# Optimization experiments

Measured on AMD Instinct MI355X. Metric: run time of the kernel, lower is better.

Reference implementation:

```python
import jax, jax.numpy as jnp
import numpy as np


def setup_inputs() -> dict:
    key = jax.random.key(0)
    bs, n_heads, ch, length = 4, 8, 64, 2048
    width = 3 * n_heads * ch  # 1536
    qkv = jax.random.normal(key, (bs, width, length), dtype=jnp.float32)
    return {"qkv": qkv, "n_heads": n_heads}


def reference(qkv, n_heads):
    bs, width, length = qkv.shape
    ch = width // (3 * n_heads)
    # reshape to (bs*heads, 3*ch, length) then split into q, k, v of (B, ch, L)
    qkv_r = qkv.reshape(bs * n_heads, 3 * ch, length)
    q, k, v = qkv_r[:, :ch], qkv_r[:, ch:2 * ch], qkv_r[:, 2 * ch:]
    scale = ch ** (-0.5)
    # weight = bmm(q^T, k) * scale -> (B, L_q, L_k)
    weight = jnp.einsum('bct,bcs->bts', q, k) * scale
    weight = jax.nn.softmax(weight.astype(jnp.float32), axis=-1).astype(qkv.dtype)
    # a = bmm(v, weight^T) -> (B, ch, L)
    a = jnp.einsum('bcs,bts->bct', v, weight)
    return a.reshape(bs, n_heads * ch, length)
```

## Files before the change

kernel.cpp:

```cpp
#include <hip/hip_runtime.h>

typedef __bf16 bf16;
typedef __attribute__((ext_vector_type(8)))  __bf16 bf16x8;
typedef __attribute__((ext_vector_type(16))) float  f32x16;

#define LEN   2048
#define CH    64
#define HEADS 32

union PackU { unsigned u[4]; bf16x8 v; };

static __device__ inline unsigned pack2(float lo, float hi) {
  union { bf16 h[2]; unsigned u; } p;
  p.h[0] = (bf16)lo; p.h[1] = (bf16)hi;
  return p.u;
}

static __device__ inline void async_cp16(const bf16* g, bf16* l) {
  __builtin_amdgcn_global_load_lds(
      (const __attribute__((address_space(1))) void*)g,
      (__attribute__((address_space(3))) void*)l, 16, 0, 0);
}

__global__ __launch_bounds__(256) void prep_kernel(const float* __restrict__ qkv,
                                                   bf16* __restrict__ ws) {
  __shared__ float tile[64][65];
  const int tIdx = blockIdx.x;
  const int g    = blockIdx.y;
  const int tid  = threadIdx.x;
  const int s0   = tIdx * 64;
  const float* K = qkv + (g * 192 + 64)  * LEN;
  const float* V = qkv + (g * 192 + 128) * LEN;

  {
    const int c0 = tid >> 6, s = tid & 63;
#pragma unroll
    for (int i = 0; i < 16; ++i) {
      const int c = c0 + i * 4;
      tile[c][s] = K[c * LEN + s0 + s];
    }
  }
  __syncthreads();

  bf16* dst = ws + ((size_t)g * 32 + tIdx) * 8192;
#pragma unroll
  for (int it = 0; it < 2; ++it) {
    const int c2  = tid + it * 256;
    const int row = c2 >> 3, cx = c2 & 7;
    const int cb  = (cx ^ (row & 7)) * 8;
    bf16x8 o;
#pragma unroll
    for (int j = 0; j < 8; ++j) o[j] = (bf16)tile[cb + j][row];
    *(bf16x8*)(dst + c2 * 8) = o;
  }
#pragma unroll
  for (int it = 0; it < 2; ++it) {
    const int c2  = tid + it * 256;
    const int row = c2 >> 3, k8 = c2 & 7;
    const int pa  = 32 * (k8 >> 2) + 8 * ((k8 >> 1) & 1) + 4 * (k8 & 1);
    const float* src = V + row * LEN + s0 + pa;
    const float4 a = *(const float4*)src;
    const float4 b = *(const float4*)(src + 16);
    bf16x8 o;
    o[0] = (bf16)a.x; o[1] = (bf16)a.y; o[2] = (bf16)a.z; o[3] = (bf16)a.w;
    o[4] = (bf16)b.x; o[5] = (bf16)b.y; o[6] = (bf16)b.z; o[7] = (bf16)b.w;
    *(bf16x8*)(dst + 4096 + c2 * 8) = o;
  }
}

__global__ __launch_bounds__(256, 2) void attn_kernel(const float* __restrict__ qkv,
                                                      const bf16* __restrict__ ws,
                                                      float* __restrict__ out) {
  __shared__ __align__(16) unsigned char lds_raw[35392];
  bf16* stg = (bf16*)lds_raw;

  const int tid  = threadIdx.x;
  const int lane = tid & 63;
  const int w    = tid >> 6;
  const int wg   = w & 1;
  const int sg   = w >> 1;
  const int n    = lane & 31;
  const int h    = lane >> 5;
  const int g    = blockIdx.x & 31;
  const int jb   = blockIdx.x >> 5;
  const int t0   = jb * 128 + wg * 64;

  const bf16* wsg    = ws + (size_t)g * (32 * 8192);
  const bf16* tiles0 = wsg + (size_t)(sg * 16) * 8192;

  auto stage = [&](int i) {
    const bf16* src = tiles0 + i * 8192;
    bf16* dstp = stg + (sg * 2 + (i & 1)) * 4096;
#pragma unroll
    for (int it = 0; it < 4; ++it) {
      const int chunk = wg * 256 + it * 64 + lane;
      async_cp16(src + chunk * 8, dstp + chunk * 8);
    }
  };
  stage(0);

  const float qs = 0.125f * 1.44269504088896340736f;
  const float* Q = qkv + g * (192 * LEN);
  bf16x8 qf[2][4];
#pragma unroll
  for (int e = 0; e < 2; ++e)
#pragma unroll
    for (int kb = 0; kb < 4; ++kb)
#pragma unroll
      for (int jj = 0; jj < 8; ++jj)
        qf[e][kb][jj] = (bf16)(Q[(kb * 16 + h * 8 + jj) * LEN + t0 + e * 32 + n] * qs);

  f32x16 o_acc[2][2];
#pragma unroll
  for (int e = 0; e < 2; ++e)
#pragma unroll
    for (int mb = 0; mb < 2; ++mb)
#pragma unroll
      for (int r = 0; r < 16; ++r) o_acc[e][mb][r] = 0.f;
  float l_acc[2] = {0.f, 0.f};

  for (int i = 0; i < 16; ++i) {
    __syncthreads();
    if (i < 15) stage(i + 1);

    const bf16* vt = tiles0 + i * 8192 + 4096;
    bf16x8 vf[4][2];
#pragma unroll
    for (int kbs = 0; kbs < 4; ++kbs)
#pragma unroll
      for (int mbo = 0; mbo < 2; ++mbo)
        vf[kbs][mbo] = *(const bf16x8*)(vt + (mbo * 32 + n) * 64 + (kbs * 2 + h) * 8);

    const bf16* ktl = stg + (sg * 2 + (i & 1)) * 4096;

    f32x16 sf[2][2];
#pragma unroll
    for (int e = 0; e < 2; ++e)
#pragma unroll
      for (int mb = 0; mb < 2; ++mb)
#pragma unroll
        for (int r = 0; r < 16; ++r) sf[e][mb][r] = 0.f;
#pragma unroll
    for (int kb = 0; kb < 4; ++kb)
#pragma unroll
      for (int mb = 0; mb < 2; ++mb) {
        const bf16x8 a = *(const bf16x8*)(ktl + (mb * 32 + n) * 64 + (((kb * 2 + h) ^ (n & 7)) * 8));
        sf[0][mb] = __builtin_amdgcn_mfma_f32_32x32x16_bf16(a, qf[0][kb], sf[0][mb], 0, 0, 0);
        sf[1][mb] = __builtin_amdgcn_mfma_f32_32x32x16_bf16(a, qf[1][kb], sf[1][mb], 0, 0, 0);
      }

    PackU frag[2][4];
#pragma unroll
    for (int e = 0; e < 2; ++e) {
      float ls = 0.f;
#pragma unroll
      for (int mb = 0; mb < 2; ++mb)
#pragma unroll
        for (int u = 0; u < 4; ++u) {
          const float p0 = __builtin_amdgcn_exp2f(sf[e][mb][4 * u + 0]);
          const float p1 = __builtin_amdgcn_exp2f(sf[e][mb][4 * u + 1]);
          const float p2 = __builtin_amdgcn_exp2f(sf[e][mb][4 * u + 2]);
          const float p3 = __builtin_amdgcn_exp2f(sf[e][mb][4 * u + 3]);
          ls += (p0 + p1) + (p2 + p3);
          const int kb   = 2 * mb + (u & 1);
          const int base = 2 * (u >> 1);
          frag[e][kb].u[base]     = pack2(p0, p1);
          frag[e][kb].u[base + 1] = pack2(p2, p3);
        }
      l_acc[e] += ls;
    }

#pragma unroll
    for (int kbs = 0; kbs < 4; ++kbs)
#pragma unroll
      for (int mbo = 0; mbo < 2; ++mbo) {
        o_acc[0][mbo] = __builtin_amdgcn_mfma_f32_32x32x16_bf16(vf[kbs][mbo], frag[0][kbs].v, o_acc[0][mbo], 0, 0, 0);
        o_acc[1][mbo] = __builtin_amdgcn_mfma_f32_32x32x16_bf16(vf[kbs][mbo], frag[1][kbs].v, o_acc[1][mbo], 0, 0, 0);
      }
  }

  float lt[2];
#pragma unroll
  for (int e = 0; e < 2; ++e) lt[e] = l_acc[e] + __shfl_xor(l_acc[e], 32);

  float* ebuf = (float*)lds_raw;
  float* lbuf = (float*)(lds_raw + 34816);

  __syncthreads();
  if (sg == 1) {
#pragma unroll
    for (int e = 0; e < 2; ++e)
#pragma unroll
      for (int mbo = 0; mbo < 2; ++mbo)
#pragma unroll
        for (int u = 0; u < 4; ++u) {
          float4 st;
          st.x = o_acc[e][mbo][4 * u + 0];
          st.y = o_acc[e][mbo][4 * u + 1];
          st.z = o_acc[e][mbo][4 * u + 2];
          st.w = o_acc[e][mbo][4 * u + 3];
          *(float4*)&ebuf[wg * 4352 + (e * 32 + n) * 68 + mbo * 32 + 8 * u + 4 * h] = st;
        }
    if (h == 0) {
      lbuf[wg * 64 + n]      = lt[0];
      lbuf[wg * 64 + 32 + n] = lt[1];
    }
  }
  __syncthreads();
  if (sg == 0) {
    float inv[2];
#pragma unroll
    for (int e = 0; e < 2; ++e) inv[e] = 1.0f / (lt[e] + lbuf[wg * 64 + e * 32 + n]);
    float* og = out + g * (CH * LEN);
#pragma unroll
    for (int e = 0; e < 2; ++e)
#pragma unroll
      for (int mbo = 0; mbo < 2; ++mbo)
#pragma unroll
        for (int u = 0; u < 4; ++u) {
          const float4 q = *(const float4*)&ebuf[wg * 4352 + (e * 32 + n) * 68 + mbo * 32 + 8 * u + 4 * h];
          const float r0 = (o_acc[e][mbo][4 * u + 0] + q.x) * inv[e];
          const float r1 = (o_acc[e][mbo][4 * u + 1] + q.y) * inv[e];
          const float r2 = (o_acc[e][mbo][4 * u + 2] + q.z) * inv[e];
          const float r3 = (o_acc[e][mbo][4 * u + 3] + q.w) * inv[e];
          const int cb = mbo * 32 + 8 * u + 4 * h;
          og[(cb + 0) * LEN + t0 + e * 32 + n] = r0;
          og[(cb + 1) * LEN + t0 + e * 32 + n] = r1;
          og[(cb + 2) * LEN + t0 + e * 32 + n] = r2;
          og[(cb + 3) * LEN + t0 + e * 32 + n] = r3;
        }
  }
}

extern "C" void kernel_launch(void* const* d_in, const int* in_sizes, int n_in,
                              void* d_out, int out_size, void* d_ws, size_t ws_size,
                              hipStream_t stream) {
  const float* qkv = (const float*)d_in[0];
  float* out = (float*)d_out;
  bf16* ws = (bf16*)d_ws;

  prep_kernel<<<dim3(32, HEADS), 256, 0, stream>>>(qkv, ws);
  attn_kernel<<<dim3(512), 256, 0, stream>>>(qkv, ws, out);
}
```

Baseline: 128.7 us.

## Load K fragments directly from global memory, dropping LDS staging and barriers

```diff
diff --git a/kernel.cpp b/kernel.cpp
--- a/kernel.cpp
+++ b/kernel.cpp
@@ -14,12 +14,6 @@
   union { bf16 h[2]; unsigned u; } p;
   p.h[0] = (bf16)lo; p.h[1] = (bf16)hi;
   return p.u;
-}
-
-static __device__ inline void async_cp16(const bf16* g, bf16* l) {
-  __builtin_amdgcn_global_load_lds(
-      (const __attribute__((address_space(1))) void*)g,
-      (__attribute__((address_space(3))) void*)l, 16, 0, 0);
 }
 
 __global__ __launch_bounds__(256) void prep_kernel(const float* __restrict__ qkv,
@@ -47,10 +41,9 @@
   for (int it = 0; it < 2; ++it) {
     const int c2  = tid + it * 256;
     const int row = c2 >> 3, cx = c2 & 7;
-    const int cb  = (cx ^ (row & 7)) * 8;
     bf16x8 o;
 #pragma unroll
-    for (int j = 0; j < 8; ++j) o[j] = (bf16)tile[cb + j][row];
+    for (int j = 0; j < 8; ++j) o[j] = (bf16)tile[cx * 8 + j][row];
     *(bf16x8*)(dst + c2 * 8) = o;
   }
 #pragma unroll
@@ -71,8 +64,7 @@
 __global__ __launch_bounds__(256, 2) void attn_kernel(const float* __restrict__ qkv,
                                                       const bf16* __restrict__ ws,
                                                       float* __restrict__ out) {
-  __shared__ __align__(16) unsigned char lds_raw[35392];
-  bf16* stg = (bf16*)lds_raw;
+  __shared__ __align__(16) unsigned char lds_raw[35328];
 
   const int tid  = threadIdx.x;
   const int lane = tid & 63;
@@ -85,19 +77,8 @@
   const int jb   = blockIdx.x >> 5;
   const int t0   = jb * 128 + wg * 64;
 
-  const bf16* wsg    = ws + (size_t)g * (32 * 8192);
-  const bf16* tiles0 = wsg + (size_t)(sg * 16) * 8192;
-
-  auto stage = [&](int i) {
-    const bf16* src = tiles0 + i * 8192;
-    bf16* dstp = stg + (sg * 2 + (i & 1)) * 4096;
-#pragma unroll
-    for (int it = 0; it < 4; ++it) {
-      const int chunk = wg * 256 + it * 64 + lane;
-      async_cp16(src + chunk * 8, dstp + chunk * 8);
-    }
-  };
-  stage(0);
+  const bf16* tiles0 = ws + (size_t)g * (32 * 8192) + (size_t)(sg * 16) * 8192;
+  const int laneoff = n * 64 + h * 8;
 
   const float qs = 0.125f * 1.44269504088896340736f;
   const float* Q = qkv + g * (192 * LEN);
@@ -110,43 +91,42 @@
       for (int jj = 0; jj < 8; ++jj)
         qf[e][kb][jj] = (bf16)(Q[(kb * 16 + h * 8 + jj) * LEN + t0 + e * 32 + n] * qs);
 
+  f32x16 zf;
+#pragma unroll
+  for (int r = 0; r < 16; ++r) zf[r] = 0.f;
+
   f32x16 o_acc[2][2];
 #pragma unroll
   for (int e = 0; e < 2; ++e)
 #pragma unroll
-    for (int mb = 0; mb < 2; ++mb)
-#pragma unroll
-      for (int r = 0; r < 16; ++r) o_acc[e][mb][r] = 0.f;
+    for (int mb = 0; mb < 2; ++mb) o_acc[e][mb] = zf;
   float l_acc[2] = {0.f, 0.f};
 
   for (int i = 0; i < 16; ++i) {
-    __syncthreads();
-    if (i < 15) stage(i + 1);
-
-    const bf16* vt = tiles0 + i * 8192 + 4096;
-    bf16x8 vf[4][2];
-#pragma unroll
-    for (int kbs = 0; kbs < 4; ++kbs)
-#pragma unroll
-      for (int mbo = 0; mbo < 2; ++mbo)
-        vf[kbs][mbo] = *(const bf16x8*)(vt + (mbo * 32 + n) * 64 + (kbs * 2 + h) * 8);
-
-    const bf16* ktl = stg + (sg * 2 + (i & 1)) * 4096;
+    const bf16* tb = tiles0 + i * 8192 + laneoff;
+
+    bf16x8 kf[4][2], vf[4][2];
+#pragma unroll
+    for (int kb = 0; kb < 4; ++kb)
+#pragma unroll
+      for (int mb = 0; mb < 2; ++mb)
+        kf[kb][mb] = *(const bf16x8*)(tb + mb * 2048 + kb * 16);
+#pragma unroll
+    for (int kb = 0; kb < 4; ++kb)
+#pragma unroll
+      for (int mb = 0; mb < 2; ++mb)
+        vf[kb][mb] = *(const bf16x8*)(tb + 4096 + mb * 2048 + kb * 16);
 
     f32x16 sf[2][2];
 #pragma unroll
     for (int e = 0; e < 2; ++e)
 #pragma unroll
-      for (int mb = 0; mb < 2; ++mb)
-#pragma unroll
-        for (int r = 0; r < 16; ++r) sf[e][mb][r] = 0.f;
-#pragma unroll
-    for (int kb = 0; kb < 4; ++kb)
-#pragma unroll
       for (int mb = 0; mb < 2; ++mb) {
-        const bf16x8 a = *(const bf16x8*)(ktl + (mb * 32 + n) * 64 + (((kb * 2 + h) ^ (n & 7)) * 8));
-        sf[0][mb] = __builtin_amdgcn_mfma_f32_32x32x16_bf16(a, qf[0][kb], sf[0][mb], 0, 0, 0);
-        sf[1][mb] = __builtin_amdgcn_mfma_f32_32x32x16_bf16(a, qf[1][kb], sf[1][mb], 0, 0, 0);
+        f32x16 acc = __builtin_amdgcn_mfma_f32_32x32x16_bf16(kf[0][mb], qf[e][0], zf, 0, 0, 0);
+#pragma unroll
+        for (int kb = 1; kb < 4; ++kb)
+          acc = __builtin_amdgcn_mfma_f32_32x32x16_bf16(kf[kb][mb], qf[e][kb], acc, 0, 0, 0);
+        sf[e][mb] = acc;
       }
 
     PackU frag[2][4];
```

Result: slower. 151.2 us (+17.5%).

## Split key dimension across four wave-pairs with 512-thread blocks and serial reduction

Applied to the files above, without the earlier changes.

```diff
diff --git a/kernel.cpp b/kernel.cpp
--- a/kernel.cpp
+++ b/kernel.cpp
@@ -68,10 +68,10 @@
   }
 }
 
-__global__ __launch_bounds__(256, 2) void attn_kernel(const float* __restrict__ qkv,
+__global__ __launch_bounds__(512, 4) void attn_kernel(const float* __restrict__ qkv,
                                                       const bf16* __restrict__ ws,
                                                       float* __restrict__ out) {
-  __shared__ __align__(16) unsigned char lds_raw[35392];
+  __shared__ __align__(16) unsigned char lds_raw[65536];
   bf16* stg = (bf16*)lds_raw;
 
   const int tid  = threadIdx.x;
@@ -86,14 +86,14 @@
   const int t0   = jb * 128 + wg * 64;
 
   const bf16* wsg    = ws + (size_t)g * (32 * 8192);
-  const bf16* tiles0 = wsg + (size_t)(sg * 16) * 8192;
+  const bf16* tiles0 = wsg + (size_t)(sg * 8) * 8192;
 
   auto stage = [&](int i) {
     const bf16* src = tiles0 + i * 8192;
     bf16* dstp = stg + (sg * 2 + (i & 1)) * 4096;
 #pragma unroll
     for (int it = 0; it < 4; ++it) {
-      const int chunk = wg * 256 + it * 64 + lane;
+      const int chunk = it * 128 + wg * 64 + lane;
       async_cp16(src + chunk * 8, dstp + chunk * 8);
     }
   };
@@ -110,18 +110,20 @@
       for (int jj = 0; jj < 8; ++jj)
         qf[e][kb][jj] = (bf16)(Q[(kb * 16 + h * 8 + jj) * LEN + t0 + e * 32 + n] * qs);
 
+  f32x16 zf;
+#pragma unroll
+  for (int r = 0; r < 16; ++r) zf[r] = 0.f;
+
   f32x16 o_acc[2][2];
 #pragma unroll
   for (int e = 0; e < 2; ++e)
 #pragma unroll
-    for (int mb = 0; mb < 2; ++mb)
-#pragma unroll
-      for (int r = 0; r < 16; ++r) o_acc[e][mb][r] = 0.f;
+    for (int mb = 0; mb < 2; ++mb) o_acc[e][mb] = zf;
   float l_acc[2] = {0.f, 0.f};
 
-  for (int i = 0; i < 16; ++i) {
+  for (int i = 0; i < 8; ++i) {
     __syncthreads();
-    if (i < 15) stage(i + 1);
+    if (i < 7) stage(i + 1);
 
     const bf16* vt = tiles0 + i * 8192 + 4096;
     bf16x8 vf[4][2];
@@ -137,16 +139,15 @@
 #pragma unroll
     for (int e = 0; e < 2; ++e)
 #pragma unroll
-      for (int mb = 0; mb < 2; ++mb)
-#pragma unroll
-        for (int r = 0; r < 16; ++r) sf[e][mb][r] = 0.f;
-#pragma unroll
-    for (int kb = 0; kb < 4; ++kb)
-#pragma unroll
       for (int mb = 0; mb < 2; ++mb) {
-        const bf16x8 a = *(const bf16x8*)(ktl + (mb * 32 + n) * 64 + (((kb * 2 + h) ^ (n & 7)) * 8));
-        sf[0][mb] = __builtin_amdgcn_mfma_f32_32x32x16_bf16(a, qf[0][kb], sf[0][mb], 0, 0, 0);
-        sf[1][mb] = __builtin_amdgcn_mfma_f32_32x32x16_bf16(a, qf[1][kb], sf[1][mb], 0, 0, 0);
+        const bf16x8 a0 = *(const bf16x8*)(ktl + (mb * 32 + n) * 64 + ((h ^ (n & 7)) * 8));
+        f32x16 acc = __builtin_amdgcn_mfma_f32_32x32x16_bf16(a0, qf[e][0], zf, 0, 0, 0);
+#pragma unroll
+        for (int kb = 1; kb < 4; ++kb) {
+          const bf16x8 a = *(const bf16x8*)(ktl + (mb * 32 + n) * 64 + (((kb * 2 + h) ^ (n & 7)) * 8));
+          acc = __builtin_amdgcn_mfma_f32_32x32x16_bf16(a, qf[e][kb], acc, 0, 0, 0);
+        }
+        sf[e][mb] = acc;
       }
 
     PackU frag[2][4];
@@ -186,31 +187,51 @@
   float* ebuf = (float*)lds_raw;
   float* lbuf = (float*)(lds_raw + 34816);
 
-  __syncthreads();
-  if (sg == 1) {
-#pragma unroll
-    for (int e = 0; e < 2; ++e)
-#pragma unroll
-      for (int mbo = 0; mbo < 2; ++mbo)
-#pragma unroll
-        for (int u = 0; u < 4; ++u) {
-          float4 st;
-          st.x = o_acc[e][mbo][4 * u + 0];
-          st.y = o_acc[e][mbo][4 * u + 1];
-          st.z = o_acc[e][mbo][4 * u + 2];
-          st.w = o_acc[e][mbo][4 * u + 3];
-          *(float4*)&ebuf[wg * 4352 + (e * 32 + n) * 68 + mbo * 32 + 8 * u + 4 * h] = st;
-        }
-    if (h == 0) {
-      lbuf[wg * 64 + n]      = lt[0];
-      lbuf[wg * 64 + 32 + n] = lt[1];
-    }
-  }
-  __syncthreads();
+#pragma unroll
+  for (int r = 1; r < 4; ++r) {
+    __syncthreads();
+    if (sg == r) {
+#pragma unroll
+      for (int e = 0; e < 2; ++e)
+#pragma unroll
+        for (int mbo = 0; mbo < 2; ++mbo)
+#pragma unroll
+          for (int u = 0; u < 4; ++u) {
+            float4 st;
+            st.x = o_acc[e][mbo][4 * u + 0];
+            st.y = o_acc[e][mbo][4 * u + 1];
+            st.z = o_acc[e][mbo][4 * u + 2];
+            st.w = o_acc[e][mbo][4 * u + 3];
+            *(float4*)&ebuf[wg * 4352 + (e * 32 + n) * 68 + mbo * 32 + 8 * u + 4 * h] = st;
+          }
+      if (h == 0) {
+        lbuf[wg * 64 + n]      = lt[0];
+        lbuf[wg * 64 + 32 + n] = lt[1];
+      }
+    }
+    __syncthreads();
+    if (sg == 0) {
+#pragma unroll
+      for (int e = 0; e < 2; ++e) {
+        lt[e] += lbuf[wg * 64 + e * 32 + n];
+#pragma unroll
+        for (int mbo = 0; mbo < 2; ++mbo)
+#pragma unroll
+          for (int u = 0; u < 4; ++u) {
+            const float4 q = *(const float4*)&ebuf[wg * 4352 + (e * 32 + n) * 68 + mbo * 32 + 8 * u + 4 * h];
+            o_acc[e][mbo][4 * u + 0] += q.x;
+            o_acc[e][mbo][4 * u + 1] += q.y;
+            o_acc[e][mbo][4 * u + 2] += q.z;
+            o_acc[e][mbo][4 * u + 3] += q.w;
+          }
+      }
+    }
+  }
+
   if (sg == 0) {
     float inv[2];
 #pragma unroll
-    for (int e = 0; e < 2; ++e) inv[e] = 1.0f / (lt[e] + lbuf[wg * 64 + e * 32 + n]);
+    for (int e = 0; e < 2; ++e) inv[e] = 1.0f / lt[e];
     float* og = out + g * (CH * LEN);
 #pragma unroll
     for (int e = 0; e < 2; ++e)
@@ -218,16 +239,11 @@
       for (int mbo = 0; mbo < 2; ++mbo)
 #pragma unroll
         for (int u = 0; u < 4; ++u) {
-          const float4 q = *(const float4*)&ebuf[wg * 4352 + (e * 32 + n) * 68 + mbo * 32 + 8 * u + 4 * h];
-          const float r0 = (o_acc[e][mbo][4 * u + 0] + q.x) * inv[e];
-          const float r1 = (o_acc[e][mbo][4 * u + 1] + q.y) * inv[e];
-          const float r2 = (o_acc[e][mbo][4 * u + 2] + q.z) * inv[e];
-          const float r3 = (o_acc[e][mbo][4 * u + 3] + q.w) * inv[e];
           const int cb = mbo * 32 + 8 * u + 4 * h;
-          og[(cb + 0) * LEN + t0 + e * 32 + n] = r0;
-          og[(cb + 1) * LEN + t0 + e * 32 + n] = r1;
-          og[(cb + 2) * LEN + t0 + e * 32 + n] = r2;
-          og[(cb + 3) * LEN + t0 + e * 32 + n] = r3;
+          og[(cb + 0) * LEN + t0 + e * 32 + n] = o_acc[e][mbo][4 * u + 0] * inv[e];
+          og[(cb + 1) * LEN + t0 + e * 32 + n] = o_acc[e][mbo][4 * u + 1] * inv[e];
+          og[(cb + 2) * LEN + t0 + e * 32 + n] = o_acc[e][mbo][4 * u + 2] * inv[e];
+          og[(cb + 3) * LEN + t0 + e * 32 + n] = o_acc[e][mbo][4 * u + 3] * inv[e];
         }
   }
 }
@@ -240,5 +256,5 @@
   bf16* ws = (bf16*)d_ws;
 
   prep_kernel<<<dim3(32, HEADS), 256, 0, stream>>>(qkv, ws);
-  attn_kernel<<<dim3(512), 256, 0, stream>>>(qkv, ws, out);
-}
+  attn_kernel<<<dim3(512), 512, 0, stream>>>(qkv, ws, out);
+}
```

Result: slower. 434.4 us (+237.5%).
